# Kernel tuning notes

Measured on AMD Instinct MI355X. Metric: run time of the kernel, lower is better.

## Reference

```python
import jax, jax.numpy as jnp
import numpy as np

EPS = 1e-06

def feature_map(x):
    # elu(x) + 1
    return jax.nn.elu(x) + 1.0

def setup_inputs() -> dict:
    key = jax.random.key(0)
    kq, kk, kv = jax.random.split(key, 3)
    N, L, S, H, D = 8, 8192, 8192, 8, 32
    queries = jax.random.normal(kq, (N, L, H, D), dtype=jnp.float32)
    keys = jax.random.normal(kk, (N, S, H, D), dtype=jnp.float32)
    values = jax.random.normal(kv, (N, S, H, D), dtype=jnp.float32)
    return {"queries": queries, "keys": keys, "values": values}

def reference(queries, keys, values):
    # Linear attention ("Transformers are RNNs"), faithful to forward_linear.
    Q = feature_map(queries)          # [N, L, H, D]
    K = feature_map(keys)             # [N, S, H, D]
    v_length = values.shape[1]
    vals = values / v_length          # [N, S, H, Dv]
    KV = jnp.einsum('nshd,nshv->nhdv', K, vals)            # [N, H, D, Dv]
    Z = 1.0 / (jnp.einsum('nlhd,nhd->nlh', Q, K.sum(axis=1)) + EPS)  # [N, L, H]
    out = jnp.einsum('nlhd,nhdv,nlh->nlhv', Q, KV, Z) * v_length     # [N, L, H, Dv]
    return out
```

## Files before the change

### kernel.cpp

```cpp
#include <hip/hip_runtime.h>


#define L_Q 8192
#define S_K 8192
#define N_HEAD 8
#define DIM 32
#define RS (N_HEAD * DIM)
#define EPSV 1e-6f

#define NPAIR 64
#define WSFLOATS (NPAIR * 1056)

__device__ __forceinline__ float fmap(float x) {
    return x > 0.0f ? x + 1.0f : __expf(x);
}

#define CHUNKS 16
#define SROWS (S_K / CHUNKS)
#define SKP 36

__global__ __launch_bounds__(256) void kv_kernel(const float* __restrict__ K,
                                                 const float* __restrict__ V,
                                                 float* __restrict__ ws)
{
    __shared__ float sK[32][SKP];
    __shared__ float sV[32][SKP];
    __shared__ float sred[4][64][16];
    __shared__ float sredk[4][32];

    const int pair = blockIdx.y;
    const int n = pair >> 3, h = pair & 7;
    const int t = threadIdx.x;
    const int w = t >> 6;
    const int l = t & 63;
    const int g = l >> 4;
    const int i = l & 15;
    const int db = i >> 2;
    const int vb = i & 3;

    const int isV = (t >= 128);
    const int st = t & 127;
    const int srow = st >> 3;
    const int scol = (st & 7) * 4;
    const float* __restrict__ src = isV ? V : K;
    float* sdst = isV ? &sV[0][0] : &sK[0][0];

    const size_t base = ((size_t)n * S_K + (size_t)blockIdx.x * SROWS) * RS
                      + (size_t)h * DIM;

    float acc[8][8];
    float ksum[8];
    #pragma unroll
    for (int a = 0; a < 8; ++a) {
        ksum[a] = 0.0f;
        #pragma unroll
        for (int b = 0; b < 8; ++b) acc[a][b] = 0.0f;
    }

    const int myrow = g * 4 + w;

    for (int s0 = 0; s0 < SROWS; s0 += 32) {
        __syncthreads();
        #pragma unroll
        for (int rr = 0; rr < 2; ++rr) {
            const int row = srow + rr * 16;
            float4 val = *(const float4*)(src + base + (size_t)(s0 + row) * RS + scol);
            if (!isV) {
                val.x = fmap(val.x); val.y = fmap(val.y);
                val.z = fmap(val.z); val.w = fmap(val.w);
            }
            *(float4*)(sdst + row * SKP + scol) = val;
        }
        __syncthreads();
        #pragma unroll
        for (int rr = 0; rr < 2; ++rr) {
            const int r = myrow + rr * 16;
            const float4 k0 = *(const float4*)&sK[r][db * 8];
            const float4 k1 = *(const float4*)&sK[r][db * 8 + 4];
            const float4 v0 = *(const float4*)&sV[r][vb * 8];
            const float4 v1 = *(const float4*)&sV[r][vb * 8 + 4];
            const float kk[8] = {k0.x,k0.y,k0.z,k0.w,k1.x,k1.y,k1.z,k1.w};
            const float vv[8] = {v0.x,v0.y,v0.z,v0.w,v1.x,v1.y,v1.z,v1.w};
            #pragma unroll
            for (int a = 0; a < 8; ++a) {
                ksum[a] += kk[a];
                #pragma unroll
                for (int b = 0; b < 8; ++b) acc[a][b] += kk[a] * vv[b];
            }
        }
    }

    #pragma unroll
    for (int a = 0; a < 8; ++a) {
        #pragma unroll
        for (int b = 0; b < 8; ++b) {
            acc[a][b] += __shfl_xor(acc[a][b], 16);
            acc[a][b] += __shfl_xor(acc[a][b], 32);
        }
        ksum[a] += __shfl_xor(ksum[a], 16);
        ksum[a] += __shfl_xor(ksum[a], 32);
    }
    __syncthreads();
    if (l < 16) {
        #pragma unroll
        for (int a = 0; a < 8; ++a)
            #pragma unroll
            for (int b = 0; b < 8; ++b)
                sred[w][a * 8 + b][i] = acc[a][b];
        if (vb == 0) {
            #pragma unroll
            for (int a = 0; a < 8; ++a) sredk[w][db * 8 + a] = ksum[a];
        }
    }
    __syncthreads();
    float* KVp = ws + pair * 1056;
    #pragma unroll
    for (int p = t; p < 1024; p += 256) {
        const int kIdx = p >> 4, iIdx = p & 15;
        const float v = sred[0][kIdx][iIdx] + sred[1][kIdx][iIdx]
                      + sred[2][kIdx][iIdx] + sred[3][kIdx][iIdx];
        const int d  = ((iIdx >> 2) << 3) + (kIdx >> 3);
        const int vv = ((iIdx & 3) << 3) + (kIdx & 7);
        unsafeAtomicAdd(&KVp[d * DIM + vv], v);
    }
    if (t < 32) {
        const float v = sredk[0][t] + sredk[1][t] + sredk[2][t] + sredk[3][t];
        unsafeAtomicAdd(&KVp[1024 + t], v);
    }
}

#define TP 260
#define BROWS 256

__global__ __launch_bounds__(256) void out_kernel(const float* __restrict__ Q,
                                                  const float* __restrict__ ws,
                                                  float* __restrict__ out)
{
    __shared__ float sQt[DIM][TP];
    __shared__ float sKV[DIM][DIM];
    __shared__ float sKs[DIM];

    const int pair = blockIdx.y;
    const int n = pair >> 3, h = pair & 7;
    const int t = threadIdx.x;
    const int w = t >> 6, l = t & 63;
    const int vb = l & 3;
    const int rb = l >> 2;

    const float* wp = ws + pair * 1056;
    for (int p = t; p < 1024; p += 256) (&sKV[0][0])[p] = wp[p];
    if (t < DIM) sKs[t] = wp[1024 + t];

    const int lrow = t >> 5;
    const int lcol = t & 31;
    const size_t qbase = ((size_t)n * L_Q + (size_t)blockIdx.x * BROWS) * RS
                       + (size_t)h * DIM;

    #pragma unroll
    for (int rr = 0; rr < BROWS / 8; ++rr) {
        const int row = lrow + rr * 8;
        sQt[lcol][row] = fmap(Q[qbase + (size_t)row * RS + lcol]);
    }
    __syncthreads();

    const int rowbase = w * 64 + rb * 4;
    float acc[4][8];
    float den[4] = {0.0f, 0.0f, 0.0f, 0.0f};
    #pragma unroll
    for (int j = 0; j < 4; ++j)
        #pragma unroll
        for (int b = 0; b < 8; ++b) acc[j][b] = 0.0f;

    #pragma unroll
    for (int d = 0; d < DIM; ++d) {
        const float4 q4 = *(const float4*)&sQt[d][rowbase];
        const float ksd = sKs[d];
        const float4 c0 = *(const float4*)&sKV[d][vb * 8];
        const float4 c1 = *(const float4*)&sKV[d][vb * 8 + 4];
        const float qq[4] = {q4.x, q4.y, q4.z, q4.w};
        const float cc[8] = {c0.x,c0.y,c0.z,c0.w,c1.x,c1.y,c1.z,c1.w};
        #pragma unroll
        for (int j = 0; j < 4; ++j) {
            den[j] += qq[j] * ksd;
            #pragma unroll
            for (int b = 0; b < 8; ++b) acc[j][b] += qq[j] * cc[b];
        }
    }

    #pragma unroll
    for (int j = 0; j < 4; ++j) {
        const float z = 1.0f / (den[j] + EPSV);
        const size_t ob = qbase + (size_t)(rowbase + j) * RS + vb * 8;
        float4 o0, o1;
        o0.x = acc[j][0] * z; o0.y = acc[j][1] * z;
        o0.z = acc[j][2] * z; o0.w = acc[j][3] * z;
        o1.x = acc[j][4] * z; o1.y = acc[j][5] * z;
        o1.z = acc[j][6] * z; o1.w = acc[j][7] * z;
        *(float4*)(out + ob) = o0;
        *(float4*)(out + ob + 4) = o1;
    }
}

extern "C" void kernel_launch(void* const* d_in, const int* in_sizes, int n_in,
                              void* d_out, int out_size, void* d_ws, size_t ws_size,
                              hipStream_t stream)
{
    const float* Q = (const float*)d_in[0];
    const float* K = (const float*)d_in[1];
    const float* V = (const float*)d_in[2];
    float* outp = (float*)d_out;
    float* ws = (float*)d_ws;

    hipMemsetAsync(d_ws, 0, WSFLOATS * sizeof(float), stream);

    dim3 gA(CHUNKS, NPAIR);
    kv_kernel<<<gA, 256, 0, stream>>>(K, V, ws);

    dim3 gB(L_Q / BROWS, NPAIR);
    out_kernel<<<gB, 256, 0, stream>>>(Q, ws, outp);
}
```

Before: 253.4 us.

## Prefetch K/V per-wave without block barriers and shrink output tiles

The KV kernel now has each wave stage its own 8-row slice of K and V in private shared memory. It prefetches the next float4 into registers, which removes the two block-wide barriers per iteration. It also doubles the S chunk count for more blocks, unions the staging and reduction shared memory, and adds occupancy hints. The output kernel halves rows per block, gives each thread a 4x4 output tile, and loads Q with float4 reads, trading more atomics and blocks for better latency hiding and coalescing.

```diff
diff --git a/kernel.cpp b/kernel.cpp
--- a/kernel.cpp
+++ b/kernel.cpp
@@ -3,11 +3,9 @@
 
 #define L_Q 8192
 #define S_K 8192
-#define N_HEAD 8
 #define DIM 32
-#define RS (N_HEAD * DIM)
+#define RS 256
 #define EPSV 1e-6f
-
 #define NPAIR 64
 #define WSFLOATS (NPAIR * 1056)
 
@@ -15,19 +13,21 @@
     return x > 0.0f ? x + 1.0f : __expf(x);
 }
 
-#define CHUNKS 16
+#define CHUNKS 32
 #define SROWS (S_K / CHUNKS)
+#define A_ITERS (SROWS / 32)
 #define SKP 36
 
-__global__ __launch_bounds__(256) void kv_kernel(const float* __restrict__ K,
-                                                 const float* __restrict__ V,
-                                                 float* __restrict__ ws)
+union SmemA {
+    struct { float K[4][8][SKP]; float V[4][8][SKP]; } st;
+    struct { float red[4][64][16]; float redk[4][32]; } rd;
+};
+
+__global__ __launch_bounds__(256, 5) void kv_kernel(const float* __restrict__ Kg,
+                                                    const float* __restrict__ Vg,
+                                                    float* __restrict__ ws)
 {
-    __shared__ float sK[32][SKP];
-    __shared__ float sV[32][SKP];
-    __shared__ float sred[4][64][16];
-    __shared__ float sredk[4][32];
-
+    __shared__ SmemA sm;
     const int pair = blockIdx.y;
     const int n = pair >> 3, h = pair & 7;
     const int t = threadIdx.x;
@@ -38,15 +38,12 @@
     const int db = i >> 2;
     const int vb = i & 3;
 
-    const int isV = (t >= 128);
-    const int st = t & 127;
-    const int srow = st >> 3;
-    const int scol = (st & 7) * 4;
-    const float* __restrict__ src = isV ? V : K;
-    float* sdst = isV ? &sV[0][0] : &sK[0][0];
+    const int srow = l >> 3;
+    const int scol = (l & 7) * 4;
 
     const size_t base = ((size_t)n * S_K + (size_t)blockIdx.x * SROWS) * RS
                       + (size_t)h * DIM;
+    size_t gaddr = base + (size_t)(w * 8 + srow) * RS + scol;
 
     float acc[8][8];
     float ksum[8];
@@ -57,24 +54,25 @@
         for (int b = 0; b < 8; ++b) acc[a][b] = 0.0f;
     }
 
-    const int myrow = g * 4 + w;
-
-    for (int s0 = 0; s0 < SROWS; s0 += 32) {
-        __syncthreads();
+    float4 pK = *(const float4*)(Kg + gaddr);
+    float4 pV = *(const float4*)(Vg + gaddr);
+
+    float (*sK)[SKP] = sm.st.K[w];
+    float (*sV)[SKP] = sm.st.V[w];
+
+    for (int it = 0; it < A_ITERS; ++it) {
+        float4 a = pK;
+        a.x = fmap(a.x); a.y = fmap(a.y); a.z = fmap(a.z); a.w = fmap(a.w);
+        *(float4*)(&sK[srow][scol]) = a;
+        *(float4*)(&sV[srow][scol]) = pV;
+        if (it + 1 < A_ITERS) {
+            gaddr += (size_t)32 * RS;
+            pK = *(const float4*)(Kg + gaddr);
+            pV = *(const float4*)(Vg + gaddr);
+        }
         #pragma unroll
         for (int rr = 0; rr < 2; ++rr) {
-            const int row = srow + rr * 16;
-            float4 val = *(const float4*)(src + base + (size_t)(s0 + row) * RS + scol);
-            if (!isV) {
-                val.x = fmap(val.x); val.y = fmap(val.y);
-                val.z = fmap(val.z); val.w = fmap(val.w);
-            }
-            *(float4*)(sdst + row * SKP + scol) = val;
-        }
-        __syncthreads();
-        #pragma unroll
-        for (int rr = 0; rr < 2; ++rr) {
-            const int r = myrow + rr * 16;
+            const int r = 2 * g + rr;
             const float4 k0 = *(const float4*)&sK[r][db * 8];
             const float4 k1 = *(const float4*)&sK[r][db * 8 + 4];
             const float4 v0 = *(const float4*)&sV[r][vb * 8];
@@ -82,10 +80,10 @@
             const float kk[8] = {k0.x,k0.y,k0.z,k0.w,k1.x,k1.y,k1.z,k1.w};
             const float vv[8] = {v0.x,v0.y,v0.z,v0.w,v1.x,v1.y,v1.z,v1.w};
             #pragma unroll
-            for (int a = 0; a < 8; ++a) {
-                ksum[a] += kk[a];
+            for (int a2 = 0; a2 < 8; ++a2) {
+                ksum[a2] += kk[a2];
                 #pragma unroll
-                for (int b = 0; b < 8; ++b) acc[a][b] += kk[a] * vv[b];
+                for (int b2 = 0; b2 < 8; ++b2) acc[a2][b2] += kk[a2] * vv[b2];
             }
         }
     }
@@ -106,10 +104,10 @@
         for (int a = 0; a < 8; ++a)
             #pragma unroll
             for (int b = 0; b < 8; ++b)
-                sred[w][a * 8 + b][i] = acc[a][b];
+                sm.rd.red[w][a * 8 + b][i] = acc[a][b];
         if (vb == 0) {
             #pragma unroll
-            for (int a = 0; a < 8; ++a) sredk[w][db * 8 + a] = ksum[a];
+            for (int a = 0; a < 8; ++a) sm.rd.redk[w][db * 8 + a] = ksum[a];
         }
     }
     __syncthreads();
@@ -117,24 +115,25 @@
     #pragma unroll
     for (int p = t; p < 1024; p += 256) {
         const int kIdx = p >> 4, iIdx = p & 15;
-        const float v = sred[0][kIdx][iIdx] + sred[1][kIdx][iIdx]
-                      + sred[2][kIdx][iIdx] + sred[3][kIdx][iIdx];
+        const float v = sm.rd.red[0][kIdx][iIdx] + sm.rd.red[1][kIdx][iIdx]
+                      + sm.rd.red[2][kIdx][iIdx] + sm.rd.red[3][kIdx][iIdx];
         const int d  = ((iIdx >> 2) << 3) + (kIdx >> 3);
         const int vv = ((iIdx & 3) << 3) + (kIdx & 7);
         unsafeAtomicAdd(&KVp[d * DIM + vv], v);
     }
     if (t < 32) {
-        const float v = sredk[0][t] + sredk[1][t] + sredk[2][t] + sredk[3][t];
+        const float v = sm.rd.redk[0][t] + sm.rd.redk[1][t]
+                      + sm.rd.redk[2][t] + sm.rd.redk[3][t];
         unsafeAtomicAdd(&KVp[1024 + t], v);
     }
 }
 
-#define TP 260
-#define BROWS 256
-
-__global__ __launch_bounds__(256) void out_kernel(const float* __restrict__ Q,
-                                                  const float* __restrict__ ws,
-                                                  float* __restrict__ out)
+#define BROWS 128
+#define TP 132
+
+__global__ __launch_bounds__(256, 8) void out_kernel(const float* __restrict__ Q,
+                                                     const float* __restrict__ ws,
+                                                     float* __restrict__ out)
 {
     __shared__ float sQt[DIM][TP];
     __shared__ float sKV[DIM][DIM];
@@ -144,60 +143,61 @@
     const int n = pair >> 3, h = pair & 7;
     const int t = threadIdx.x;
     const int w = t >> 6, l = t & 63;
-    const int vb = l & 3;
-    const int rb = l >> 2;
+    const int vb = l & 7;
+    const int rb = l >> 3;
 
     const float* wp = ws + pair * 1056;
     for (int p = t; p < 1024; p += 256) (&sKV[0][0])[p] = wp[p];
     if (t < DIM) sKs[t] = wp[1024 + t];
 
-    const int lrow = t >> 5;
-    const int lcol = t & 31;
     const size_t qbase = ((size_t)n * L_Q + (size_t)blockIdx.x * BROWS) * RS
                        + (size_t)h * DIM;
 
-    #pragma unroll
-    for (int rr = 0; rr < BROWS / 8; ++rr) {
-        const int row = lrow + rr * 8;
-        sQt[lcol][row] = fmap(Q[qbase + (size_t)row * RS + lcol]);
+    {
+        const int r = t >> 1;
+        const int half = (t & 1) * 16;
+        const float* qp = Q + qbase + (size_t)r * RS + half;
+        #pragma unroll
+        for (int j = 0; j < 4; ++j) {
+            const float4 v = *(const float4*)(qp + j * 4);
+            sQt[half + j * 4 + 0][r] = fmap(v.x);
+            sQt[half + j * 4 + 1][r] = fmap(v.y);
+            sQt[half + j * 4 + 2][r] = fmap(v.z);
+            sQt[half + j * 4 + 3][r] = fmap(v.w);
+        }
     }
     __syncthreads();
 
-    const int rowbase = w * 64 + rb * 4;
-    float acc[4][8];
+    const int rowbase = w * 32 + rb * 4;
+    float acc[4][4];
     float den[4] = {0.0f, 0.0f, 0.0f, 0.0f};
     #pragma unroll
     for (int j = 0; j < 4; ++j)
         #pragma unroll
-        for (int b = 0; b < 8; ++b) acc[j][b] = 0.0f;
+        for (int b = 0; b < 4; ++b) acc[j][b] = 0.0f;
 
     #pragma unroll
     for (int d = 0; d < DIM; ++d) {
         const float4 q4 = *(const float4*)&sQt[d][rowbase];
         const float ksd = sKs[d];
-        const float4 c0 = *(const float4*)&sKV[d][vb * 8];
-        const float4 c1 = *(const float4*)&sKV[d][vb * 8 + 4];
+        const float4 c = *(const float4*)&sKV[d][vb * 4];
         const float qq[4] = {q4.x, q4.y, q4.z, q4.w};
-        const float cc[8] = {c0.x,c0.y,c0.z,c0.w,c1.x,c1.y,c1.z,c1.w};
+        const float cc[4] = {c.x, c.y, c.z, c.w};
         #pragma unroll
         for (int j = 0; j < 4; ++j) {
             den[j] += qq[j] * ksd;
             #pragma unroll
-            for (int b = 0; b < 8; ++b) acc[j][b] += qq[j] * cc[b];
+            for (int b = 0; b < 4; ++b) acc[j][b] += qq[j] * cc[b];
         }
     }
 
     #pragma unroll
     for (int j = 0; j < 4; ++j) {
         const float z = 1.0f / (den[j] + EPSV);
-        const size_t ob = qbase + (size_t)(rowbase + j) * RS + vb * 8;
-        float4 o0, o1;
-        o0.x = acc[j][0] * z; o0.y = acc[j][1] * z;
-        o0.z = acc[j][2] * z; o0.w = acc[j][3] * z;
-        o1.x = acc[j][4] * z; o1.y = acc[j][5] * z;
-        o1.z = acc[j][6] * z; o1.w = acc[j][7] * z;
-        *(float4*)(out + ob) = o0;
-        *(float4*)(out + ob + 4) = o1;
+        float4 o;
+        o.x = acc[j][0] * z; o.y = acc[j][1] * z;
+        o.z = acc[j][2] * z; o.w = acc[j][3] * z;
+        *(float4*)(out + qbase + (size_t)(rowbase + j) * RS + vb * 4) = o;
     }
 }
 
```

Measured after the change: 274.4 us. +8.3%, slower.
